# Optimization experiments

Measured on AMD Instinct MI355X. Metric: run time of the kernel, lower is better.

Reference implementation:

```python
import jax, jax.numpy as jnp
import numpy as np
from jax import lax

B, T = 16, 8192
CIN, HALF, F = 2, 1, 256
KS, NL, NB, TB = 3, 3, 10, 5.0
PROJ = HALF * (3 * NB - 1)


def setup_inputs() -> dict:
    key = jax.random.key(0)
    ks = jax.random.split(key, 16)
    inp = {
        'x': jax.random.normal(ks[0], (B, T, CIN), dtype=jnp.float32),
        'x_mask': jnp.ones((B, T, 1), dtype=jnp.float32),
        'w_pre': jax.random.normal(ks[1], (HALF, F)) * 0.1,
        'b_pre': jnp.zeros((F,)),
        'dw_k': jax.random.normal(ks[2], (NL, KS, 1, F)) * 0.1,   # depthwise kernels [L,k,1,C]
        'dw_b': jnp.zeros((NL, F)),
        'w11': jax.random.normal(ks[3], (NL, F, F)) * 0.05,
        'b11': jnp.zeros((NL, F)),
        'ln1_g': jnp.ones((NL, F)), 'ln1_b': jnp.zeros((NL, F)),
        'ln2_g': jnp.ones((NL, F)), 'ln2_b': jnp.zeros((NL, F)),
        'w_proj': jax.random.normal(ks[4], (F, PROJ)) * 0.05,
        'b_proj': jnp.zeros((PROJ,)),
    }
    return inp


def _layer_norm(x, g, b, eps=1e-5):
    m = jnp.mean(x, axis=-1, keepdims=True)
    v = jnp.mean(jnp.square(x - m), axis=-1, keepdims=True)
    return (x - m) * lax.rsqrt(v + eps) * g + b


def _rq_spline(x, uw, uh, ud, tail_bound, mbw=1e-3, mbh=1e-3, md=1e-3):
    # x: [B,c,T]; uw,uh: [B,c,T,K]; ud: [B,c,T,K-1]. tails='linear'.
    K = uw.shape[-1]
    const = float(np.log(np.expm1(1.0 - md)))  # boundary derivative == 1
    ud = jnp.pad(ud, [(0, 0)] * (ud.ndim - 1) + [(1, 1)], constant_values=const)
    inside = (x >= -tail_bound) & (x <= tail_bound)

    w = jax.nn.softmax(uw, axis=-1)
    w = mbw + (1.0 - mbw * K) * w
    cw = jnp.pad(jnp.cumsum(w, axis=-1), [(0, 0)] * (w.ndim - 1) + [(1, 0)])
    cw = 2.0 * tail_bound * cw - tail_bound
    cw = cw.at[..., 0].set(-tail_bound).at[..., -1].set(tail_bound)
    w = jnp.diff(cw, axis=-1)

    hgt = jax.nn.softmax(uh, axis=-1)
    hgt = mbh + (1.0 - mbh * K) * hgt
    ch = jnp.pad(jnp.cumsum(hgt, axis=-1), [(0, 0)] * (hgt.ndim - 1) + [(1, 0)])
    ch = 2.0 * tail_bound * ch - tail_bound
    ch = ch.at[..., 0].set(-tail_bound).at[..., -1].set(tail_bound)
    hgt = jnp.diff(ch, axis=-1)

    d = md + jax.nn.softplus(ud)  # [B,c,T,K+1]

    xc = jnp.clip(x, -tail_bound, tail_bound)
    idx = jnp.clip(jnp.sum((xc[..., None] >= cw).astype(jnp.int32), axis=-1) - 1, 0, K - 1)

    def g1(a, i):
        return jnp.take_along_axis(a, i[..., None], axis=-1)[..., 0]

    icw, ibw = g1(cw, idx), g1(w, idx)
    ich, ibh = g1(ch, idx), g1(hgt, idx)
    delta = ibh / ibw
    dk, dk1 = g1(d, idx), g1(d, idx + 1)

    th = (xc - icw) / ibw
    th1m = th * (1.0 - th)
    denom = delta + (dk + dk1 - 2.0 * delta) * th1m
    num = ibh * (delta * th * th + dk * th1m)
    yv = ich + num / denom
    dnum = jnp.square(delta) * (dk1 * th * th + 2.0 * delta * th1m + dk * jnp.square(1.0 - th))
    lad = jnp.log(dnum) - 2.0 * jnp.log(denom)

    y = jnp.where(inside, yv, x)
    lad = jnp.where(inside, lad, jnp.zeros_like(lad))
    return y, lad


def reference(x, x_mask, w_pre, b_pre, dw_k, dw_b, w11, b11,
              ln1_g, ln1_b, ln2_g, ln2_b, w_proj, b_proj):
    half = w_pre.shape[0]
    F_ = w_pre.shape[1]
    nl, ks = dw_k.shape[0], dw_k.shape[1]
    x0, x1 = x[..., :half], x[..., half:]

    h = x0 @ w_pre + b_pre  # pre 1x1 conv, [B,T,F]
    for i in range(nl):  # DDSConv
        dil = ks ** i
        y = lax.conv_general_dilated(h * x_mask, dw_k[i], (1,), 'SAME',
                                     rhs_dilation=(dil,),
                                     dimension_numbers=('NWC', 'WIO', 'NWC'),
                                     feature_group_count=F_) + dw_b[i]
        y = jax.nn.gelu(_layer_norm(y, ln1_g[i], ln1_b[i]), approximate=False)
        y = y @ w11[i] + b11[i]
        y = jax.nn.gelu(_layer_norm(y, ln2_g[i], ln2_b[i]), approximate=False)
        h = h + y
    h = h * x_mask
    h = (h @ w_proj + b_proj) * x_mask  # [B,T,half*(3*NB-1)]

    b_, t_ = x.shape[0], x.shape[1]
    nb = (h.shape[-1] // half + 1) // 3
    h = h.reshape(b_, t_, half, 3 * nb - 1).transpose(0, 2, 1, 3)  # [B,half,T,3NB-1]
    x1t = jnp.swapaxes(x1, 1, 2)  # [B,half,T]

    scale = 1.0 / np.sqrt(F_)
    uw = h[..., :nb] * scale
    uh = h[..., nb:2 * nb] * scale
    ud = h[..., 2 * nb:]

    y1, lad = _rq_spline(x1t, uw, uh, ud, TB)
    x1o = jnp.swapaxes(y1, 1, 2)           # [B,T,half]
    lad_t = jnp.swapaxes(lad, 1, 2)        # [B,T,half]

    xo = jnp.concatenate([x0, x1o], axis=-1) * x_mask
    logdet = jnp.sum(lad_t * x_mask, axis=(2, 1))
    return xo, logdet
```

## Files before the change

### kernel.cpp

```cpp
#include <hip/hip_runtime.h>
#include <hip/hip_bf16.h>
#include <cmath>

#define BB 16
#define TT 8192
#define MM (BB*TT)
#define FF 256
#define TBF 5.0f
#define PROJN 29

typedef __attribute__((ext_vector_type(8))) short short8;
typedef __attribute__((ext_vector_type(4))) float f32x4;

__device__ __forceinline__ float gelu_fast(float x){
    const float x2 = x*x;
    const float v  = x*fmaf(0.07135481627f, x2, 1.595769122f);
    const float e  = __expf(-v);
    return x*__builtin_amdgcn_rcpf(1.0f + e);
}
__device__ __forceinline__ float softplusf_(float v){
    return fmaxf(v,0.0f) + log1pf(__expf(-fabsf(v)));
}
__device__ __forceinline__ unsigned pack2bf(float a, float b){
    __hip_bfloat16 ha = __float2bfloat16(a);
    __hip_bfloat16 hb = __float2bfloat16(b);
    const unsigned ua = *reinterpret_cast<const unsigned short*>(&ha);
    const unsigned ub = *reinterpret_cast<const unsigned short*>(&hb);
    return ua | (ub<<16);
}
__device__ __forceinline__ float bf2f(unsigned short u){
    unsigned v = ((unsigned)u)<<16;
    return *reinterpret_cast<float*>(&v);
}
__device__ __forceinline__ float4 unpack4(uint2 q){
    float4 f;
    f.x = bf2f((unsigned short)(q.x&0xffff)); f.y = bf2f((unsigned short)(q.x>>16));
    f.z = bf2f((unsigned short)(q.y&0xffff)); f.w = bf2f((unsigned short)(q.y>>16));
    return f;
}

__global__ __launch_bounds__(256) void wprep_kernel(
    const float* __restrict__ w11, const float* __restrict__ wproj,
    __hip_bfloat16* __restrict__ wimg, __hip_bfloat16* __restrict__ wpimg)
{
    if(blockIdx.x < 24){
        const int layer = blockIdx.x>>3, kc = blockIdx.x&7;
        const float* __restrict__ w = w11 + (size_t)layer*FF*FF;
        __hip_bfloat16* __restrict__ o = wimg + (size_t)layer*81920 + kc*10240;
        for(int i=threadIdx.x; i<10240; i+=256){
            const int n = i/40, kp = i - n*40;
            const float v = (kp<32) ? w[(size_t)(kc*32+kp)*FF + n] : 0.0f;
            o[i] = __float2bfloat16(v);
        }
    } else {
        const int kc = blockIdx.x - 24;
        __hip_bfloat16* __restrict__ o = wpimg + (size_t)kc*1280;
        for(int i=threadIdx.x; i<1280; i+=256){
            const int n = i/40, kp = i - n*40;
            const float v = (kp<32 && n<PROJN) ? wproj[(size_t)(kc*32+kp)*PROJN + n] : 0.0f;
            o[i] = __float2bfloat16(v);
        }
    }
}

__global__ __launch_bounds__(256,4) void layer_kernel(
    const __hip_bfloat16* __restrict__ hbin, __hip_bfloat16* __restrict__ hbout,
    const float* __restrict__ xsrc,
    const float* __restrict__ w_pre, const float* __restrict__ b_pre,
    const float* __restrict__ mask,
    const float* __restrict__ dwk, const float* __restrict__ dwb,
    const float* __restrict__ g1, const float* __restrict__ b1,
    const __hip_bfloat16* __restrict__ wimgL, const float* __restrict__ b11,
    const float* __restrict__ g2, const float* __restrict__ b2,
    const int dil, const int pre_mode)
{
    __shared__ __hip_bfloat16 ytile[32][260];
    __shared__ __hip_bfloat16 hstash[32][260];
    __shared__ float redS[32][4];
    __shared__ float redQ[32][4];
    __shared__ float stat[32][2];

    const int tid  = threadIdx.x;
    const int wave = tid>>6, lane = tid&63;
    const int l15  = lane&15, qq = lane>>4;

    int bid = blockIdx.x;
    bid = (bid&7)*((int)gridDim.x>>3) + (bid>>3);
    const int m0 = bid*32;
    const int b  = m0/TT;
    const int t0 = m0 - b*TT;
    const float* __restrict__ mrow = mask + (size_t)b*TT;

    const int f0 = lane*4;
    const float4 k0 = *(const float4*)&dwk[f0];
    const float4 k1 = *(const float4*)&dwk[FF+f0];
    const float4 k2 = *(const float4*)&dwk[2*FF+f0];
    const float4 cb = *(const float4*)&dwb[f0];
    const float4 g1v= *(const float4*)&g1[f0];
    const float4 b1v= *(const float4*)&b1[f0];
    float4 wp4, bp4;
    if(pre_mode){ wp4 = *(const float4*)&w_pre[f0]; bp4 = *(const float4*)&b_pre[f0]; }

    #pragma unroll 4
    for(int rr=0; rr<8; ++rr){
        const int r = wave*8+rr;
        const int m = m0+r, t = t0+r;
        const int okl = (t>=dil)   ? 1 : 0;
        const int okr = (t+dil<TT) ? 1 : 0;
        const int ml  = m - dil*okl;
        const int mr  = m + dil*okr;
        const float mkc = mrow[t];
        const float mkl = mrow[t - dil*okl] * (float)okl;
        const float mkr = mrow[t + dil*okr] * (float)okr;
        float4 hc, hl, hr;
        uint2 hcraw;
        if(pre_mode){
            const float xc_ = xsrc[(size_t)m *2];
            const float xl_ = xsrc[(size_t)ml*2];
            const float xr_ = xsrc[(size_t)mr*2];
            hc.x=fmaf(xc_,wp4.x,bp4.x); hc.y=fmaf(xc_,wp4.y,bp4.y);
            hc.z=fmaf(xc_,wp4.z,bp4.z); hc.w=fmaf(xc_,wp4.w,bp4.w);
            hl.x=fmaf(xl_,wp4.x,bp4.x); hl.y=fmaf(xl_,wp4.y,bp4.y);
            hl.z=fmaf(xl_,wp4.z,bp4.z); hl.w=fmaf(xl_,wp4.w,bp4.w);
            hr.x=fmaf(xr_,wp4.x,bp4.x); hr.y=fmaf(xr_,wp4.y,bp4.y);
            hr.z=fmaf(xr_,wp4.z,bp4.z); hr.w=fmaf(xr_,wp4.w,bp4.w);
            hcraw = make_uint2(pack2bf(hc.x,hc.y), pack2bf(hc.z,hc.w));
        } else {
            hcraw          = *(const uint2*)&hbin[(size_t)m *FF + f0];
            const uint2 ql = *(const uint2*)&hbin[(size_t)ml*FF + f0];
            const uint2 qr = *(const uint2*)&hbin[(size_t)mr*FF + f0];
            hc = unpack4(hcraw); hl = unpack4(ql); hr = unpack4(qr);
        }
        *(uint2*)&hstash[r][f0] = hcraw;
        float4 a;
        a.x = fmaf(hc.x*mkc, k1.x, cb.x);
        a.y = fmaf(hc.y*mkc, k1.y, cb.y);
        a.z = fmaf(hc.z*mkc, k1.z, cb.z);
        a.w = fmaf(hc.w*mkc, k1.w, cb.w);
        a.x = fmaf(hl.x*mkl, k0.x, a.x);
        a.y = fmaf(hl.y*mkl, k0.y, a.y);
        a.z = fmaf(hl.z*mkl, k0.z, a.z);
        a.w = fmaf(hl.w*mkl, k0.w, a.w);
        a.x = fmaf(hr.x*mkr, k2.x, a.x);
        a.y = fmaf(hr.y*mkr, k2.y, a.y);
        a.z = fmaf(hr.z*mkr, k2.z, a.z);
        a.w = fmaf(hr.w*mkr, k2.w, a.w);
        float s  = a.x+a.y+a.z+a.w;
        float sq = fmaf(a.x,a.x, fmaf(a.y,a.y, fmaf(a.z,a.z, a.w*a.w)));
        #pragma unroll
        for(int o=32;o>0;o>>=1){
            s  += __shfl_xor(s,o,64);
            sq += __shfl_xor(sq,o,64);
        }
        const float mean = s*(1.0f/FF);
        const float var  = fmaf(-mean, mean, sq*(1.0f/FF));
        const float rs = rsqrtf(var + 1e-5f);
        const float y0 = gelu_fast(fmaf((a.x-mean)*rs, g1v.x, b1v.x));
        const float y1 = gelu_fast(fmaf((a.y-mean)*rs, g1v.y, b1v.y));
        const float y2 = gelu_fast(fmaf((a.z-mean)*rs, g1v.z, b1v.z));
        const float y3 = gelu_fast(fmaf((a.w-mean)*rs, g1v.w, b1v.w));
        *(uint2*)&ytile[r][f0] = make_uint2(pack2bf(y0,y1), pack2bf(y2,y3));
    }

    __syncthreads();

    const int wc = wave*64;
    f32x4 acc[2][4];
    #pragma unroll
    for(int mf=0;mf<2;++mf)
        #pragma unroll
        for(int nf=0;nf<4;++nf)
            acc[mf][nf] = (f32x4){0.f,0.f,0.f,0.f};

    #pragma unroll
    for(int kc=0;kc<8;++kc){
        short8 bfv[4];
        #pragma unroll
        for(int nf=0;nf<4;++nf)
            bfv[nf] = *(const short8*)&wimgL[(size_t)kc*10240 + (wc+nf*16+l15)*40 + qq*8];
        short8 af[2];
        #pragma unroll
        for(int mf=0;mf<2;++mf)
            af[mf] = *(const short8*)&ytile[mf*16+l15][kc*32 + qq*8];
        #pragma unroll
        for(int nf=0;nf<4;++nf)
            #pragma unroll
            for(int mf=0;mf<2;++mf)
                acc[mf][nf] = __builtin_amdgcn_mfma_f32_16x16x32_bf16(af[mf], bfv[nf], acc[mf][nf], 0,0,0);
    }

    float b11c[4], g2c[4], b2c[4];
    #pragma unroll
    for(int nf=0;nf<4;++nf){
        const int col = wc + nf*16 + l15;
        b11c[nf]=b11[col]; g2c[nf]=g2[col]; b2c[nf]=b2[col];
    }
    #pragma unroll
    for(int mf=0;mf<2;++mf){
        #pragma unroll
        for(int rg=0;rg<4;++rg){
            float s=0.f, sq=0.f;
            #pragma unroll
            for(int nf=0;nf<4;++nf){
                const float v = acc[mf][nf][rg] + b11c[nf];
                s += v; sq = fmaf(v,v,sq);
            }
            #pragma unroll
            for(int o=1;o<16;o<<=1){ s += __shfl_xor(s,o,64); sq += __shfl_xor(sq,o,64); }
            if(l15==0){
                const int row = mf*16 + qq*4 + rg;
                redS[row][wave]=s; redQ[row][wave]=sq;
            }
        }
    }
    __syncthreads();
    if(tid < 32){
        const float s  = redS[tid][0]+redS[tid][1]+redS[tid][2]+redS[tid][3];
        const float q2 = redQ[tid][0]+redQ[tid][1]+redQ[tid][2]+redQ[tid][3];
        const float mean = s*(1.0f/FF);
        const float var  = fmaf(-mean, mean, q2*(1.0f/FF));
        stat[tid][0]=mean; stat[tid][1]=rsqrtf(var+1e-5f);
    }
    __syncthreads();
    #pragma unroll
    for(int mf=0;mf<2;++mf){
        #pragma unroll
        for(int rg=0;rg<4;++rg){
            const int row = mf*16 + qq*4 + rg;
            const float mean = stat[row][0], rs = stat[row][1];
            const size_t gbase = (size_t)(m0+row)*FF;
            #pragma unroll
            for(int nf=0;nf<4;++nf){
                const int col = wc + nf*16 + l15;
                const float v  = acc[mf][nf][rg] + b11c[nf];
                const float yn = fmaf((v-mean)*rs, g2c[nf], b2c[nf]);
                const float res = bf2f(*reinterpret_cast<const unsigned short*>(&hstash[row][col]));
                hbout[gbase+col] = __float2bfloat16(res + gelu_fast(yn));
            }
        }
    }
}

__global__ __launch_bounds__(256,2) void projspline_kernel(
    const __hip_bfloat16* __restrict__ hbin, const float* __restrict__ mask,
    const __hip_bfloat16* __restrict__ wpimg, const float* __restrict__ bproj,
    const float* __restrict__ x, float* __restrict__ out,
    float* __restrict__ logdet)
{
    __shared__ __hip_bfloat16 ytile[64][260];
    __shared__ float Pl[256][37];
    __shared__ float red[256];

    const int tid = threadIdx.x;
    const int wave = tid>>6, lane = tid&63;
    const int l15 = lane&15, qq = lane>>4;
    const int m0 = blockIdx.x*256;
    const int f0 = lane*4;

    const int col = (wave>>1)*16 + l15;
    const float bp = (col<PROJN)? bproj[col] : 0.0f;

    for(int ch=0; ch<4; ++ch){
        const int mc = m0 + ch*64;
        #pragma unroll 4
        for(int rr=0; rr<16; ++rr){
            const int r = wave*16+rr;
            const int m = mc+r;
            const float mk = mask[m];
            const float4 hc = unpack4(*(const uint2*)&hbin[(size_t)m*FF + f0]);
            *(uint2*)&ytile[r][f0] = make_uint2(pack2bf(hc.x*mk, hc.y*mk), pack2bf(hc.z*mk, hc.w*mk));
        }
        __syncthreads();

        const int rh = (wave&1)*32, wc2 = (wave>>1)*16;
        f32x4 acc[2];
        acc[0] = (f32x4){0.f,0.f,0.f,0.f};
        acc[1] = (f32x4){0.f,0.f,0.f,0.f};
        #pragma unroll
        for(int kc=0;kc<8;++kc){
            const short8 bfv = *(const short8*)&wpimg[(size_t)kc*1280 + (wc2+l15)*40 + qq*8];
            #pragma unroll
            for(int mf=0;mf<2;++mf){
                const short8 af = *(const short8*)&ytile[rh+mf*16+l15][kc*32 + qq*8];
                acc[mf] = __builtin_amdgcn_mfma_f32_16x16x32_bf16(af, bfv, acc[mf], 0,0,0);
            }
        }
        #pragma unroll
        for(int mf=0;mf<2;++mf){
            #pragma unroll
            for(int rg=0;rg<4;++rg){
                const int row = rh + mf*16 + qq*4 + rg;
                const float mk = mask[mc+row];
                Pl[ch*64+row][col] = (acc[mf][rg] + bp)*mk;
            }
        }
        __syncthreads();
    }

    const int m = m0 + tid;
    float p[29];
    #pragma unroll
    for(int j=0;j<29;++j) p[j] = Pl[tid][j];
    const float x0 = x[(size_t)m*2];
    const float x1 = x[(size_t)m*2+1];
    const float mk = mask[m];
    const float sc = 0.0625f;

    float cw[11], ch_[11], d[11];
    {
        float mx=-1e30f;
        #pragma unroll
        for(int j=0;j<10;++j) mx = fmaxf(mx, p[j]);
        float e[10]; float se=0.f;
        #pragma unroll
        for(int j=0;j<10;++j){ e[j]=__expf((p[j]-mx)*sc); se+=e[j]; }
        const float inv = __builtin_amdgcn_rcpf(se);
        float cum=0.f;
        cw[0]=-TBF;
        #pragma unroll
        for(int j=0;j<10;++j){ cum += fmaf(0.99f, e[j]*inv, 0.001f); cw[j+1]=fmaf(2.0f*TBF,cum,-TBF); }
        cw[10]=TBF;
    }
    {
        float mx=-1e30f;
        #pragma unroll
        for(int j=0;j<10;++j) mx = fmaxf(mx, p[10+j]);
        float e[10]; float se=0.f;
        #pragma unroll
        for(int j=0;j<10;++j){ e[j]=__expf((p[10+j]-mx)*sc); se+=e[j]; }
        const float inv = __builtin_amdgcn_rcpf(se);
        float cum=0.f;
        ch_[0]=-TBF;
        #pragma unroll
        for(int j=0;j<10;++j){ cum += fmaf(0.99f, e[j]*inv, 0.001f); ch_[j+1]=fmaf(2.0f*TBF,cum,-TBF); }
        ch_[10]=TBF;
    }
    d[0]=1.0f; d[10]=1.0f;
    #pragma unroll
    for(int k=1;k<10;++k) d[k] = 0.001f + softplusf_(p[19+k]);

    const bool inside = (x1>=-TBF)&&(x1<=TBF);
    const float xc = fminf(fmaxf(x1,-TBF),TBF);

    float icw=cw[0], ibw=cw[1]-cw[0], ich=ch_[0], ibh=ch_[1]-ch_[0], dk=d[0], dk1=d[1];
    #pragma unroll
    for(int j=1;j<10;++j){
        const bool sel = (xc>=cw[j]);
        icw = sel? cw[j]        : icw;
        ibw = sel? cw[j+1]-cw[j]: ibw;
        ich = sel? ch_[j]       : ich;
        ibh = sel? ch_[j+1]-ch_[j]: ibh;
        dk  = sel? d[j]         : dk;
        dk1 = sel? d[j+1]       : dk1;
    }

    const float delta = __fdividef(ibh, ibw);
    const float th = __fdividef(xc-icw, ibw);
    const float th1m = th*(1.0f-th);
    const float denom = fmaf(fmaf(-2.0f,delta,dk+dk1), th1m, delta);
    const float num = ibh*fmaf(delta*th, th, dk*th1m);
    const float rcd = __builtin_amdgcn_rcpf(denom);
    const float yv = ich + num*rcd;
    const float omt = 1.0f-th;
    const float dnum = delta*delta*(dk1*th*th + 2.0f*delta*th1m + dk*omt*omt);
    const float lad = __logf(dnum*rcd*rcd);
    const float y1 = inside? yv : x1;
    const float lv = inside? lad : 0.0f;

    out[(size_t)m*2]   = x0*mk;
    out[(size_t)m*2+1] = y1*mk;

    red[tid]=lv*mk;
    __syncthreads();
    #pragma unroll
    for(int s=128;s>0;s>>=1){ if(tid<s) red[tid]+=red[tid+s]; __syncthreads(); }
    if(tid==0) atomicAdd(&logdet[blockIdx.x>>5], red[0]);
}

__global__ __launch_bounds__(256,4) void proj_kernel(
    const __hip_bfloat16* __restrict__ hbin, const float* __restrict__ mask,
    const __hip_bfloat16* __restrict__ wpimg, const float* __restrict__ bproj,
    float* __restrict__ P)
{
    __shared__ __hip_bfloat16 ytile[64][260];
    const int tid = threadIdx.x;
    const int wave = tid>>6, lane = tid&63;
    const int l15 = lane&15, qq = lane>>4;
    const int m0 = blockIdx.x*64;
    const int f0 = lane*4;

    #pragma unroll 4
    for(int rr=0; rr<16; ++rr){
        const int r = wave*16+rr;
        const int m = m0+r;
        const float mk = mask[m];
        const float4 hc = unpack4(*(const uint2*)&hbin[(size_t)m*FF + f0]);
        *(uint2*)&ytile[r][f0] = make_uint2(pack2bf(hc.x*mk, hc.y*mk), pack2bf(hc.z*mk, hc.w*mk));
    }
    __syncthreads();

    const int rh = (wave&1)*32, wc2 = (wave>>1)*16;
    f32x4 acc[2];
    acc[0] = (f32x4){0.f,0.f,0.f,0.f};
    acc[1] = (f32x4){0.f,0.f,0.f,0.f};
    #pragma unroll
    for(int kc=0;kc<8;++kc){
        const short8 bfv = *(const short8*)&wpimg[(size_t)kc*1280 + (wc2+l15)*40 + qq*8];
        #pragma unroll
        for(int mf=0;mf<2;++mf){
            const short8 af = *(const short8*)&ytile[rh+mf*16+l15][kc*32 + qq*8];
            acc[mf] = __builtin_amdgcn_mfma_f32_16x16x32_bf16(af, bfv, acc[mf], 0,0,0);
        }
    }
    const int col = wc2 + l15;
    const float bp = (col<PROJN)? bproj[col] : 0.0f;
    #pragma unroll
    for(int mf=0;mf<2;++mf){
        #pragma unroll
        for(int rg=0;rg<4;++rg){
            const int row = rh + mf*16 + qq*4 + rg;
            const float mk = mask[m0+row];
            P[(size_t)(m0+row)*32 + col] = (acc[mf][rg] + bp)*mk;
        }
    }
}

__global__ __launch_bounds__(256) void spline_kernel(
    const float* __restrict__ P, const float* __restrict__ x,
    const float* __restrict__ mask, float* __restrict__ out,
    float* __restrict__ logdet)
{
    const int tid = threadIdx.x;
    const int m = blockIdx.x*256 + tid;
    float p[32];
    #pragma unroll
    for(int j=0;j<8;++j) ((float4*)p)[j] = ((const float4*)P)[(size_t)m*8+j];
    const float x0 = x[(size_t)m*2];
    const float x1 = x[(size_t)m*2+1];
    const float mk = mask[m];
    const float sc = 0.0625f;

    float cw[11], ch_[11], d[11];
    {
        float mx=-1e30f;
        #pragma unroll
        for(int j=0;j<10;++j) mx = fmaxf(mx, p[j]);
        float e[10]; float se=0.f;
        #pragma unroll
        for(int j=0;j<10;++j){ e[j]=__expf((p[j]-mx)*sc); se+=e[j]; }
        const float inv = __builtin_amdgcn_rcpf(se);
        float cum=0.f;
        cw[0]=-TBF;
        #pragma unroll
        for(int j=0;j<10;++j){ cum += fmaf(0.99f, e[j]*inv, 0.001f); cw[j+1]=fmaf(2.0f*TBF,cum,-TBF); }
        cw[10]=TBF;
    }
    {
        float mx=-1e30f;
        #pragma unroll
        for(int j=0;j<10;++j) mx = fmaxf(mx, p[10+j]);
        float e[10]; float se=0.f;
        #pragma unroll
        for(int j=0;j<10;++j){ e[j]=__expf((p[10+j]-mx)*sc); se+=e[j]; }
        const float inv = __builtin_amdgcn_rcpf(se);
        float cum=0.f;
        ch_[0]=-TBF;
        #pragma unroll
        for(int j=0;j<10;++j){ cum += fmaf(0.99f, e[j]*inv, 0.001f); ch_[j+1]=fmaf(2.0f*TBF,cum,-TBF); }
        ch_[10]=TBF;
    }
    d[0]=1.0f; d[10]=1.0f;
    #pragma unroll
    for(int k=1;k<10;++k) d[k] = 0.001f + softplusf_(p[19+k]);

    const bool inside = (x1>=-TBF)&&(x1<=TBF);
    const float xc = fminf(fmaxf(x1,-TBF),TBF);

    float icw=cw[0], ibw=cw[1]-cw[0], ich=ch_[0], ibh=ch_[1]-ch_[0], dk=d[0], dk1=d[1];
    #pragma unroll
    for(int j=1;j<10;++j){
        const bool sel = (xc>=cw[j]);
        icw = sel? cw[j]        : icw;
        ibw = sel? cw[j+1]-cw[j]: ibw;
        ich = sel? ch_[j]       : ich;
        ibh = sel? ch_[j+1]-ch_[j]: ibh;
        dk  = sel? d[j]         : dk;
        dk1 = sel? d[j+1]       : dk1;
    }

    const float delta = __fdividef(ibh, ibw);
    const float th = __fdividef(xc-icw, ibw);
    const float th1m = th*(1.0f-th);
    const float denom = fmaf(fmaf(-2.0f,delta,dk+dk1), th1m, delta);
    const float num = ibh*fmaf(delta*th, th, dk*th1m);
    const float rcd = __builtin_amdgcn_rcpf(denom);
    const float yv = ich + num*rcd;
    const float omt = 1.0f-th;
    const float dnum = delta*delta*(dk1*th*th + 2.0f*delta*th1m + dk*omt*omt);
    const float lad = __logf(dnum*rcd*rcd);
    const float y1 = inside? yv : x1;
    const float lv = inside? lad : 0.0f;

    out[(size_t)m*2]   = x0*mk;
    out[(size_t)m*2+1] = y1*mk;

    __shared__ float red[256];
    red[tid]=lv*mk;
    __syncthreads();
    #pragma unroll
    for(int s=128;s>0;s>>=1){ if(tid<s) red[tid]+=red[tid+s]; __syncthreads(); }
    if(tid==0) atomicAdd(&logdet[blockIdx.x>>5], red[0]);
}

extern "C" void kernel_launch(void* const* d_in, const int* in_sizes, int n_in,
                              void* d_out, int out_size, void* d_ws, size_t ws_size,
                              hipStream_t stream)
{
    const float* x      = (const float*)d_in[0];
    const float* mask   = (const float*)d_in[1];
    const float* w_pre  = (const float*)d_in[2];
    const float* b_pre  = (const float*)d_in[3];
    const float* dw_k   = (const float*)d_in[4];
    const float* dw_b   = (const float*)d_in[5];
    const float* w11    = (const float*)d_in[6];
    const float* b11    = (const float*)d_in[7];
    const float* ln1g   = (const float*)d_in[8];
    const float* ln1b   = (const float*)d_in[9];
    const float* ln2g   = (const float*)d_in[10];
    const float* ln2b   = (const float*)d_in[11];
    const float* w_proj = (const float*)d_in[12];
    const float* b_proj = (const float*)d_in[13];

    const size_t hbytes_bf16 = (size_t)MM*FF*2;
    __hip_bfloat16* h0 = (__hip_bfloat16*)d_ws;
    __hip_bfloat16* h1 = h0 + (size_t)MM*FF;
    float* outp   = (float*)d_out;
    float* logdet = outp + (size_t)MM*2;

    const size_t wimg_bytes = (size_t)3*163840 + 20480;
    __hip_bfloat16* wimg;
    const bool ws_ok = (ws_size >= 2*hbytes_bf16 + wimg_bytes);
    if(ws_ok) wimg = (__hip_bfloat16*)((char*)d_ws + 2*hbytes_bf16);
    else      wimg = (__hip_bfloat16*)d_out;
    __hip_bfloat16* wpimg = wimg + (size_t)3*81920;

    wprep_kernel<<<32, 256, 0, stream>>>(w11, w_proj, wimg, wpimg);

    layer_kernel<<<MM/32, 256, 0, stream>>>(
        (const __hip_bfloat16*)nullptr, h1, x, w_pre, b_pre, mask,
        dw_k, dw_b, ln1g, ln1b, wimg, b11, ln2g, ln2b, 1, 1);
    layer_kernel<<<MM/32, 256, 0, stream>>>(
        h1, h0, x, w_pre, b_pre, mask,
        dw_k + (size_t)3*FF, dw_b + (size_t)FF,
        ln1g + (size_t)FF, ln1b + (size_t)FF,
        wimg + (size_t)81920, b11 + (size_t)FF,
        ln2g + (size_t)FF, ln2b + (size_t)FF, 3, 0);
    layer_kernel<<<MM/32, 256, 0, stream>>>(
        h0, h1, x, w_pre, b_pre, mask,
        dw_k + (size_t)6*FF, dw_b + (size_t)2*FF,
        ln1g + (size_t)2*FF, ln1b + (size_t)2*FF,
        wimg + (size_t)2*81920, b11 + (size_t)2*FF,
        ln2g + (size_t)2*FF, ln2b + (size_t)2*FF, 9, 0);

    hipMemsetAsync(logdet, 0, BB*sizeof(float), stream);
    if(ws_ok){
        projspline_kernel<<<MM/256, 256, 0, stream>>>(h1, mask, wpimg, b_proj, x, outp, logdet);
    } else {
        float* P = (float*)d_ws;
        proj_kernel<<<MM/64, 256, 0, stream>>>(h1, mask, wpimg, b_proj, P);
        spline_kernel<<<MM/256, 256, 0, stream>>>(P, x, mask, outp, logdet);
    }
}
```

Baseline: 327.5 us.

## Drop residual LDS stash, template pre-mode, and halve projspline tile for occupancy

The layer kernel no longer stashes the residual row in LDS. It reloads the residual from global memory, or recomputes it from x in the first layer, at the epilogue. A template parameter specialises the pre-projection path, and launch bounds are raised to 8 blocks per CU. The projspline kernel processes 128 rows per block instead of 256, with smaller LDS tiles and higher launch bounds, though only half the threads run the spline stage. The aim is to cut LDS use so more blocks fit per CU, in exchange for an extra global read of the residual and lower per-block work.

```diff
diff --git a/kernel.cpp b/kernel.cpp
--- a/kernel.cpp
+++ b/kernel.cpp
@@ -63,7 +63,8 @@
     }
 }
 
-__global__ __launch_bounds__(256,4) void layer_kernel(
+template<int PRE>
+__global__ __launch_bounds__(256,8) void layer_kernel(
     const __hip_bfloat16* __restrict__ hbin, __hip_bfloat16* __restrict__ hbout,
     const float* __restrict__ xsrc,
     const float* __restrict__ w_pre, const float* __restrict__ b_pre,
@@ -72,10 +73,9 @@
     const float* __restrict__ g1, const float* __restrict__ b1,
     const __hip_bfloat16* __restrict__ wimgL, const float* __restrict__ b11,
     const float* __restrict__ g2, const float* __restrict__ b2,
-    const int dil, const int pre_mode)
+    const int dil)
 {
     __shared__ __hip_bfloat16 ytile[32][260];
-    __shared__ __hip_bfloat16 hstash[32][260];
     __shared__ float redS[32][4];
     __shared__ float redQ[32][4];
     __shared__ float stat[32][2];
@@ -99,7 +99,7 @@
     const float4 g1v= *(const float4*)&g1[f0];
     const float4 b1v= *(const float4*)&b1[f0];
     float4 wp4, bp4;
-    if(pre_mode){ wp4 = *(const float4*)&w_pre[f0]; bp4 = *(const float4*)&b_pre[f0]; }
+    if(PRE){ wp4 = *(const float4*)&w_pre[f0]; bp4 = *(const float4*)&b_pre[f0]; }
 
     #pragma unroll 4
     for(int rr=0; rr<8; ++rr){
@@ -113,8 +113,7 @@
         const float mkl = mrow[t - dil*okl] * (float)okl;
         const float mkr = mrow[t + dil*okr] * (float)okr;
         float4 hc, hl, hr;
-        uint2 hcraw;
-        if(pre_mode){
+        if(PRE){
             const float xc_ = xsrc[(size_t)m *2];
             const float xl_ = xsrc[(size_t)ml*2];
             const float xr_ = xsrc[(size_t)mr*2];
@@ -124,14 +123,11 @@
             hl.z=fmaf(xl_,wp4.z,bp4.z); hl.w=fmaf(xl_,wp4.w,bp4.w);
             hr.x=fmaf(xr_,wp4.x,bp4.x); hr.y=fmaf(xr_,wp4.y,bp4.y);
             hr.z=fmaf(xr_,wp4.z,bp4.z); hr.w=fmaf(xr_,wp4.w,bp4.w);
-            hcraw = make_uint2(pack2bf(hc.x,hc.y), pack2bf(hc.z,hc.w));
         } else {
-            hcraw          = *(const uint2*)&hbin[(size_t)m *FF + f0];
-            const uint2 ql = *(const uint2*)&hbin[(size_t)ml*FF + f0];
-            const uint2 qr = *(const uint2*)&hbin[(size_t)mr*FF + f0];
-            hc = unpack4(hcraw); hl = unpack4(ql); hr = unpack4(qr);
-        }
-        *(uint2*)&hstash[r][f0] = hcraw;
+            hc = unpack4(*(const uint2*)&hbin[(size_t)m *FF + f0]);
+            hl = unpack4(*(const uint2*)&hbin[(size_t)ml*FF + f0]);
+            hr = unpack4(*(const uint2*)&hbin[(size_t)mr*FF + f0]);
+        }
         float4 a;
         a.x = fmaf(hc.x*mkc, k1.x, cb.x);
         a.y = fmaf(hc.y*mkc, k1.y, cb.y);
@@ -189,11 +185,12 @@
                 acc[mf][nf] = __builtin_amdgcn_mfma_f32_16x16x32_bf16(af[mf], bfv[nf], acc[mf][nf], 0,0,0);
     }
 
-    float b11c[4], g2c[4], b2c[4];
+    float b11c[4], g2c[4], b2c[4], wpc[4], bpc[4];
     #pragma unroll
     for(int nf=0;nf<4;++nf){
         const int col = wc + nf*16 + l15;
         b11c[nf]=b11[col]; g2c[nf]=g2[col]; b2c[nf]=b2[col];
+        if(PRE){ wpc[nf]=w_pre[col]; bpc[nf]=b_pre[col]; }
     }
     #pragma unroll
     for(int mf=0;mf<2;++mf){
@@ -229,42 +226,48 @@
             const int row = mf*16 + qq*4 + rg;
             const float mean = stat[row][0], rs = stat[row][1];
             const size_t gbase = (size_t)(m0+row)*FF;
+            float x0r;
+            if(PRE) x0r = xsrc[(size_t)(m0+row)*2];
             #pragma unroll
             for(int nf=0;nf<4;++nf){
                 const int col = wc + nf*16 + l15;
                 const float v  = acc[mf][nf][rg] + b11c[nf];
                 const float yn = fmaf((v-mean)*rs, g2c[nf], b2c[nf]);
-                const float res = bf2f(*reinterpret_cast<const unsigned short*>(&hstash[row][col]));
+                float res;
+                if(PRE) res = fmaf(x0r, wpc[nf], bpc[nf]);
+                else    res = bf2f(*reinterpret_cast<const unsigned short*>(&hbin[gbase+col]));
                 hbout[gbase+col] = __float2bfloat16(res + gelu_fast(yn));
             }
         }
     }
 }
 
-__global__ __launch_bounds__(256,2) void projspline_kernel(
+__global__ __launch_bounds__(256,4) void projspline_kernel(
     const __hip_bfloat16* __restrict__ hbin, const float* __restrict__ mask,
     const __hip_bfloat16* __restrict__ wpimg, const float* __restrict__ bproj,
     const float* __restrict__ x, float* __restrict__ out,
     float* __restrict__ logdet)
 {
-    __shared__ __hip_bfloat16 ytile[64][260];
-    __shared__ float Pl[256][37];
+    __shared__ __hip_bfloat16 ytile[32][260];
+    __shared__ float Pl[128][33];
     __shared__ float red[256];
 
     const int tid = threadIdx.x;
     const int wave = tid>>6, lane = tid&63;
     const int l15 = lane&15, qq = lane>>4;
-    const int m0 = blockIdx.x*256;
+    const int m0 = blockIdx.x*128;
     const int f0 = lane*4;
 
-    const int col = (wave>>1)*16 + l15;
+    const int rh  = (wave&1)*16;
+    const int wc2 = (wave>>1)*16;
+    const int col = wc2 + l15;
     const float bp = (col<PROJN)? bproj[col] : 0.0f;
 
-    for(int ch=0; ch<4; ++ch){
-        const int mc = m0 + ch*64;
-        #pragma unroll 4
-        for(int rr=0; rr<16; ++rr){
-            const int r = wave*16+rr;
+    for(int chk=0; chk<4; ++chk){
+        const int mc = m0 + chk*32;
+        #pragma unroll
+        for(int rr=0; rr<8; ++rr){
+            const int r = wave*8+rr;
             const int m = mc+r;
             const float mk = mask[m];
             const float4 hc = unpack4(*(const uint2*)&hbin[(size_t)m*FF + f0]);
@@ -272,109 +275,104 @@
         }
         __syncthreads();
 
-        const int rh = (wave&1)*32, wc2 = (wave>>1)*16;
-        f32x4 acc[2];
-        acc[0] = (f32x4){0.f,0.f,0.f,0.f};
-        acc[1] = (f32x4){0.f,0.f,0.f,0.f};
+        f32x4 acc = (f32x4){0.f,0.f,0.f,0.f};
         #pragma unroll
         for(int kc=0;kc<8;++kc){
             const short8 bfv = *(const short8*)&wpimg[(size_t)kc*1280 + (wc2+l15)*40 + qq*8];
-            #pragma unroll
-            for(int mf=0;mf<2;++mf){
-                const short8 af = *(const short8*)&ytile[rh+mf*16+l15][kc*32 + qq*8];
-                acc[mf] = __builtin_amdgcn_mfma_f32_16x16x32_bf16(af, bfv, acc[mf], 0,0,0);
-            }
-        }
-        #pragma unroll
-        for(int mf=0;mf<2;++mf){
-            #pragma unroll
-            for(int rg=0;rg<4;++rg){
-                const int row = rh + mf*16 + qq*4 + rg;
-                const float mk = mask[mc+row];
-                Pl[ch*64+row][col] = (acc[mf][rg] + bp)*mk;
-            }
+            const short8 af  = *(const short8*)&ytile[rh+l15][kc*32 + qq*8];
+            acc = __builtin_amdgcn_mfma_f32_16x16x32_bf16(af, bfv, acc, 0,0,0);
+        }
+        #pragma unroll
+        for(int rg=0;rg<4;++rg){
+            const int row = rh + qq*4 + rg;
+            const float mk = mask[mc+row];
+            Pl[chk*32+row][col] = (acc[rg] + bp)*mk;
         }
         __syncthreads();
     }
 
-    const int m = m0 + tid;
-    float p[29];
-    #pragma unroll
-    for(int j=0;j<29;++j) p[j] = Pl[tid][j];
-    const float x0 = x[(size_t)m*2];
-    const float x1 = x[(size_t)m*2+1];
-    const float mk = mask[m];
-    const float sc = 0.0625f;
-
-    float cw[11], ch_[11], d[11];
-    {
-        float mx=-1e30f;
-        #pragma unroll
-        for(int j=0;j<10;++j) mx = fmaxf(mx, p[j]);
-        float e[10]; float se=0.f;
-        #pragma unroll
-        for(int j=0;j<10;++j){ e[j]=__expf((p[j]-mx)*sc); se+=e[j]; }
-        const float inv = __builtin_amdgcn_rcpf(se);
-        float cum=0.f;
-        cw[0]=-TBF;
-        #pragma unroll
-        for(int j=0;j<10;++j){ cum += fmaf(0.99f, e[j]*inv, 0.001f); cw[j+1]=fmaf(2.0f*TBF,cum,-TBF); }
-        cw[10]=TBF;
-    }
-    {
-        float mx=-1e30f;
-        #pragma unroll
-        for(int j=0;j<10;++j) mx = fmaxf(mx, p[10+j]);
-        float e[10]; float se=0.f;
-        #pragma unroll
-        for(int j=0;j<10;++j){ e[j]=__expf((p[10+j]-mx)*sc); se+=e[j]; }
-        const float inv = __builtin_amdgcn_rcpf(se);
-        float cum=0.f;
-        ch_[0]=-TBF;
-        #pragma unroll
-        for(int j=0;j<10;++j){ cum += fmaf(0.99f, e[j]*inv, 0.001f); ch_[j+1]=fmaf(2.0f*TBF,cum,-TBF); }
-        ch_[10]=TBF;
-    }
-    d[0]=1.0f; d[10]=1.0f;
-    #pragma unroll
-    for(int k=1;k<10;++k) d[k] = 0.001f + softplusf_(p[19+k]);
-
-    const bool inside = (x1>=-TBF)&&(x1<=TBF);
-    const float xc = fminf(fmaxf(x1,-TBF),TBF);
-
-    float icw=cw[0], ibw=cw[1]-cw[0], ich=ch_[0], ibh=ch_[1]-ch_[0], dk=d[0], dk1=d[1];
-    #pragma unroll
-    for(int j=1;j<10;++j){
-        const bool sel = (xc>=cw[j]);
-        icw = sel? cw[j]        : icw;
-        ibw = sel? cw[j+1]-cw[j]: ibw;
-        ich = sel? ch_[j]       : ich;
-        ibh = sel? ch_[j+1]-ch_[j]: ibh;
-        dk  = sel? d[j]         : dk;
-        dk1 = sel? d[j+1]       : dk1;
-    }
-
-    const float delta = __fdividef(ibh, ibw);
-    const float th = __fdividef(xc-icw, ibw);
-    const float th1m = th*(1.0f-th);
-    const float denom = fmaf(fmaf(-2.0f,delta,dk+dk1), th1m, delta);
-    const float num = ibh*fmaf(delta*th, th, dk*th1m);
-    const float rcd = __builtin_amdgcn_rcpf(denom);
-    const float yv = ich + num*rcd;
-    const float omt = 1.0f-th;
-    const float dnum = delta*delta*(dk1*th*th + 2.0f*delta*th1m + dk*omt*omt);
-    const float lad = __logf(dnum*rcd*rcd);
-    const float y1 = inside? yv : x1;
-    const float lv = inside? lad : 0.0f;
-
-    out[(size_t)m*2]   = x0*mk;
-    out[(size_t)m*2+1] = y1*mk;
-
-    red[tid]=lv*mk;
+    float lv_mk = 0.0f;
+    if(tid < 128){
+        const int m = m0 + tid;
+        float p[29];
+        #pragma unroll
+        for(int j=0;j<29;++j) p[j] = Pl[tid][j];
+        const float x0 = x[(size_t)m*2];
+        const float x1 = x[(size_t)m*2+1];
+        const float mk = mask[m];
+        const float sc = 0.0625f;
+
+        float cw[11], ch_[11], d[11];
+        {
+            float mx=-1e30f;
+            #pragma unroll
+            for(int j=0;j<10;++j) mx = fmaxf(mx, p[j]);
+            float e[10]; float se=0.f;
+            #pragma unroll
+            for(int j=0;j<10;++j){ e[j]=__expf((p[j]-mx)*sc); se+=e[j]; }
+            const float inv = __builtin_amdgcn_rcpf(se);
+            float cum=0.f;
+            cw[0]=-TBF;
+            #pragma unroll
+            for(int j=0;j<10;++j){ cum += fmaf(0.99f, e[j]*inv, 0.001f); cw[j+1]=fmaf(2.0f*TBF,cum,-TBF); }
+            cw[10]=TBF;
+        }
+        {
+            float mx=-1e30f;
+            #pragma unroll
+            for(int j=0;j<10;++j) mx = fmaxf(mx, p[10+j]);
+            float e[10]; float se=0.f;
+            #pragma unroll
+            for(int j=0;j<10;++j){ e[j]=__expf((p[10+j]-mx)*sc); se+=e[j]; }
+            const float inv = __builtin_amdgcn_rcpf(se);
+            float cum=0.f;
+            ch_[0]=-TBF;
+            #pragma unroll
+            for(int j=0;j<10;++j){ cum += fmaf(0.99f, e[j]*inv, 0.001f); ch_[j+1]=fmaf(2.0f*TBF,cum,-TBF); }
+            ch_[10]=TBF;
+        }
+        d[0]=1.0f; d[10]=1.0f;
+        #pragma unroll
+        for(int k=1;k<10;++k) d[k] = 0.001f + softplusf_(p[19+k]);
+
+        const bool inside = (x1>=-TBF)&&(x1<=TBF);
+        const float xc = fminf(fmaxf(x1,-TBF),TBF);
+
+        float icw=cw[0], ibw=cw[1]-cw[0], ich=ch_[0], ibh=ch_[1]-ch_[0], dk=d[0], dk1=d[1];
+        #pragma unroll
+        for(int j=1;j<10;++j){
+            const bool sel = (xc>=cw[j]);
+            icw = sel? cw[j]        : icw;
+            ibw = sel? cw[j+1]-cw[j]: ibw;
+            ich = sel? ch_[j]       : ich;
+            ibh = sel? ch_[j+1]-ch_[j]: ibh;
+            dk  = sel? d[j]         : dk;
+            dk1 = sel? d[j+1]       : dk1;
+        }
+
+        const float delta = __fdividef(ibh, ibw);
+        const float th = __fdividef(xc-icw, ibw);
+        const float th1m = th*(1.0f-th);
+        const float denom = fmaf(fmaf(-2.0f,delta,dk+dk1), th1m, delta);
+        const float num = ibh*fmaf(delta*th, th, dk*th1m);
+        const float rcd = __builtin_amdgcn_rcpf(denom);
+        const float yv = ich + num*rcd;
+        const float omt = 1.0f-th;
+        const float dnum = delta*delta*(dk1*th*th + 2.0f*delta*th1m + dk*omt*omt);
+        const float lad = __logf(dnum*rcd*rcd);
+        const float y1 = inside? yv : x1;
+        const float lv = inside? lad : 0.0f;
+
+        out[(size_t)m*2]   = x0*mk;
+        out[(size_t)m*2+1] = y1*mk;
+        lv_mk = lv*mk;
+    }
+
+    red[tid] = lv_mk;
     __syncthreads();
     #pragma unroll
     for(int s=128;s>0;s>>=1){ if(tid<s) red[tid]+=red[tid+s]; __syncthreads(); }
-    if(tid==0) atomicAdd(&logdet[blockIdx.x>>5], red[0]);
+    if(tid==0) atomicAdd(&logdet[blockIdx.x>>6], red[0]);
 }
 
 __global__ __launch_bounds__(256,4) void proj_kernel(
@@ -546,25 +544,25 @@
 
     wprep_kernel<<<32, 256, 0, stream>>>(w11, w_proj, wimg, wpimg);
 
-    layer_kernel<<<MM/32, 256, 0, stream>>>(
+    layer_kernel<1><<<MM/32, 256, 0, stream>>>(
         (const __hip_bfloat16*)nullptr, h1, x, w_pre, b_pre, mask,
-        dw_k, dw_b, ln1g, ln1b, wimg, b11, ln2g, ln2b, 1, 1);
-    layer_kernel<<<MM/32, 256, 0, stream>>>(
+        dw_k, dw_b, ln1g, ln1b, wimg, b11, ln2g, ln2b, 1);
+    layer_kernel<0><<<MM/32, 256, 0, stream>>>(
         h1, h0, x, w_pre, b_pre, mask,
         dw_k + (size_t)3*FF, dw_b + (size_t)FF,
         ln1g + (size_t)FF, ln1b + (size_t)FF,
         wimg + (size_t)81920, b11 + (size_t)FF,
-        ln2g + (size_t)FF, ln2b + (size_t)FF, 3, 0);
-    layer_kernel<<<MM/32, 256, 0, stream>>>(
+        ln2g + (size_t)FF, ln2b + (size_t)FF, 3);
+    layer_kernel<0><<<MM/32, 256, 0, stream>>>(
         h0, h1, x, w_pre, b_pre, mask,
         dw_k + (size_t)6*FF, dw_b + (size_t)2*FF,
         ln1g + (size_t)2*FF, ln1b + (size_t)2*FF,
         wimg + (size_t)2*81920, b11 + (size_t)2*FF,
-        ln2g + (size_t)2*FF, ln2b + (size_t)2*FF, 9, 0);
+        ln2g + (size_t)2*FF, ln2b + (size_t)2*FF, 9);
 
     hipMemsetAsync(logdet, 0, BB*sizeof(float), stream);
     if(ws_ok){
-        projspline_kernel<<<MM/256, 256, 0, stream>>>(h1, mask, wpimg, b_proj, x, outp, logdet);
+        projspline_kernel<<<MM/128, 256, 0, stream>>>(h1, mask, wpimg, b_proj, x, outp, logdet);
     } else {
         float* P = (float*)d_ws;
         proj_kernel<<<MM/64, 256, 0, stream>>>(h1, mask, wpimg, b_proj, P);
```

New measurement: 751.3 us. +129.4%, slower.
